# Performance work log

Hardware: AMD Instinct MI355X
Metric: run time of the kernel (lower is better)

Reference implementation:

```python
import jax, jax.numpy as jnp
import numpy as np

DIM = 768
HEADS = 12
HEAD_DIM = DIM // HEADS
B, N = 8, 1024


def setup_inputs() -> dict:
    key = jax.random.key(0)
    ks = jax.random.split(key, 5)
    x = jax.random.normal(ks[0], (B, N, DIM), dtype=jnp.float32)
    shared_rel_pos = jax.random.normal(ks[1], (HEADS, N, N), dtype=jnp.float32)
    qkv_w = jax.random.normal(ks[2], (3 * DIM, DIM), dtype=jnp.float32) * (DIM ** -0.5)
    proj_w = jax.random.normal(ks[3], (DIM, DIM), dtype=jnp.float32) * (DIM ** -0.5)
    proj_b = jnp.zeros((DIM,), dtype=jnp.float32)
    return {"x": x, "shared_rel_pos": shared_rel_pos, "qkv_w": qkv_w,
            "proj_w": proj_w, "proj_b": proj_b}


def reference(x, shared_rel_pos, qkv_w, proj_w, proj_b):
    Bt, Nt, C = x.shape
    scale = HEAD_DIM ** -0.5
    # qkv: Linear(dim, 3*dim, bias=False) -> (B, N, 3, H, hd) -> (3, B, H, N, hd)
    qkv = jnp.einsum('bnc,oc->bno', x, qkv_w)
    qkv = qkv.reshape(Bt, Nt, 3, HEADS, HEAD_DIM).transpose(2, 0, 3, 1, 4)
    q, k, v = qkv[0], qkv[1], qkv[2]
    # scaled dot-product attention with shared relative-position bias
    attn = jnp.einsum('bhqd,bhkd->bhqk', q, k) * scale
    attn = attn + shared_rel_pos[None]  # broadcast over batch
    attn = jax.nn.softmax(attn, axis=-1)
    out = jnp.einsum('bhqk,bhkd->bhqd', attn, v)
    out = out.transpose(0, 2, 1, 3).reshape(Bt, Nt, C)
    return jnp.einsum('bnc,oc->bno', out, proj_w) + proj_b
```

## Files before the change

kernel.cpp:

```cpp
#include <hip/hip_runtime.h>
#include <hip/hip_bf16.h>
#include <stdint.h>

#define HEADS 12
#define HD 64
#define SEQ 1024
#define CDIM 768

typedef __attribute__((ext_vector_type(8))) short bfrag;
typedef __attribute__((ext_vector_type(4))) float facc;

__device__ __forceinline__ ushort f2bf(float f) {
    union { float f; uint32_t u; } v; v.f = f;
    uint32_t u = v.u;
    uint32_t r = (u + 0x7FFFu + ((u >> 16) & 1u)) >> 16;
    return (ushort)r;
}
__device__ __forceinline__ float h2f(uint32_t u16) {
    union { _Float16 h; ushort u; } c; c.u = (ushort)u16; return (float)c.h;
}

__global__ void cvt_f32_bf16(const float* __restrict__ s, ushort* __restrict__ d, int n) {
    int i = (blockIdx.x * 256 + threadIdx.x) * 4;
    if (i + 3 < n) {
        float4 v = *(const float4*)(s + i);
        ushort4 o;
        o.x = f2bf(v.x); o.y = f2bf(v.y); o.z = f2bf(v.z); o.w = f2bf(v.w);
        *(ushort4*)(d + i) = o;
    }
}

__global__ void cvt_f32_f16(const float* __restrict__ s, ushort* __restrict__ d, int n) {
    int i = (blockIdx.x * 256 + threadIdx.x) * 4;
    if (i + 3 < n) {
        float4 v = *(const float4*)(s + i);
        union { _Float16 h; ushort u; } c0, c1, c2, c3;
        c0.h = (_Float16)v.x; c1.h = (_Float16)v.y;
        c2.h = (_Float16)v.z; c3.h = (_Float16)v.w;
        ushort4 o = {c0.u, c1.u, c2.u, c3.u};
        *(ushort4*)(d + i) = o;
    }
}

#define GLOAD16(gsrc, ldst) \
    __builtin_amdgcn_global_load_lds((const __attribute__((address_space(1))) uint32_t*)(gsrc), \
                                     (__attribute__((address_space(3))) uint32_t*)(ldst), 16, 0, 0)

template<int EPI>
__global__ __launch_bounds__(256) void gemm_nt(
    const ushort* __restrict__ A, const ushort* __restrict__ Bm,
    ushort* __restrict__ qb, ushort* __restrict__ kb, ushort* __restrict__ vb,
    const float* __restrict__ projb, float* __restrict__ out)
{
    __shared__ ushort As[128 * 32];
    __shared__ ushort Bs[128 * 32];
    const int t = threadIdx.x;
    const int w = t >> 6, l = t & 63;
    const int wm = w >> 1, wn = w & 1;
    const int lr = l & 15, lg = l >> 4;
    const int m0 = blockIdx.x * 128;
    const int o0 = blockIdx.y * 128;

    facc acc[4][4] = {};

    const int srow = w * 16 + (l >> 2);
    const int scol = (l & 3) * 8;
    const ushort* Ag = A + (size_t)(m0 + srow) * CDIM + scol;
    const ushort* Bg = Bm + (size_t)(o0 + srow) * CDIM + scol;

    for (int k0 = 0; k0 < CDIM; k0 += 32) {
        __syncthreads();
        GLOAD16(Ag + k0,             As + w * 512);
        GLOAD16(Ag + 64 * CDIM + k0, As + 2048 + w * 512);
        GLOAD16(Bg + k0,             Bs + w * 512);
        GLOAD16(Bg + 64 * CDIM + k0, Bs + 2048 + w * 512);
        __syncthreads();
        bfrag af[4], bf[4];
#pragma unroll
        for (int m = 0; m < 4; ++m)
            af[m] = *(const bfrag*)&As[(wm * 64 + m * 16 + lr) * 32 + lg * 8];
#pragma unroll
        for (int n = 0; n < 4; ++n)
            bf[n] = *(const bfrag*)&Bs[(wn * 64 + n * 16 + lr) * 32 + lg * 8];
#pragma unroll
        for (int m = 0; m < 4; ++m)
#pragma unroll
            for (int n = 0; n < 4; ++n)
                acc[m][n] = __builtin_amdgcn_mfma_f32_16x16x32_bf16(af[m], bf[n], acc[m][n], 0, 0, 0);
    }

    if (EPI == 0) {
        const int tsel = o0 / CDIM;
        const int h_base = (o0 % CDIM) / 64;
        ushort* dst = (tsel == 0) ? qb : ((tsel == 1) ? kb : vb);
        const float scl = (tsel == 0) ? 0.125f : 1.0f;
#pragma unroll
        for (int m = 0; m < 4; ++m) {
            int grow = m0 + wm * 64 + m * 16 + lg * 4;
#pragma unroll
            for (int n = 0; n < 4; ++n) {
                int h = h_base + wn;
                int d = n * 16 + lr;
#pragma unroll
                for (int r = 0; r < 4; ++r) {
                    int row = grow + r;
                    int b = row >> 10, nn = row & 1023;
                    dst[(((size_t)(b * HEADS + h)) * SEQ + nn) * HD + d] = f2bf(acc[m][n][r] * scl);
                }
            }
        }
    } else {
#pragma unroll
        for (int m = 0; m < 4; ++m) {
            int grow = m0 + wm * 64 + m * 16 + lg * 4;
#pragma unroll
            for (int n = 0; n < 4; ++n) {
                int o = o0 + wn * 64 + n * 16 + lr;
                float bias = projb[o];
#pragma unroll
                for (int r = 0; r < 4; ++r)
                    out[(size_t)(grow + r) * CDIM + o] = acc[m][n][r] + bias;
            }
        }
    }
}

__global__ __launch_bounds__(256, 3) void attn_kernel(
    const ushort* __restrict__ qbuf, const ushort* __restrict__ kbuf,
    const ushort* __restrict__ vbuf, const ushort* __restrict__ biash,
    ushort* __restrict__ attn_out)
{
    __shared__ ushort Ks[64 * 72];
    __shared__ ushort Vt[64 * 72];
    __shared__ ushort Ps[4][32 * 72];

    const int t = threadIdx.x;
    const int w = t >> 6, l = t & 63;
    const int lr = l & 15, lg = l >> 4;

    const int bid = blockIdx.x;
    const int lid = (bid & 7) * 96 + (bid >> 3);
    const int h  = lid >> 6;
    const int qt = (lid >> 3) & 7;
    const int b  = lid & 7;

    const int q0 = qt * 128;
    const size_t headoff = (size_t)(b * HEADS + h) * SEQ * HD;
    const int qrb = q0 + w * 32;

    bfrag aQ[2][2];
#pragma unroll
    for (int n = 0; n < 2; ++n) {
        const ushort* Qp = qbuf + headoff + (size_t)(qrb + n * 16 + lr) * HD;
        aQ[n][0] = *(const bfrag*)(Qp + lg * 8);
        aQ[n][1] = *(const bfrag*)(Qp + 32 + lg * 8);
    }

    float mrun[2] = {-1e30f, -1e30f}, lrun[2] = {0.0f, 0.0f};
    facc Ov[2][4] = {};

    const ushort* bprow[2];
#pragma unroll
    for (int n = 0; n < 2; ++n)
        bprow[n] = biash + ((size_t)h * SEQ + qrb + n * 16 + lr) * SEQ;

    const int krow = t >> 3, kc = (t & 7) * 8;
    const int p2 = t & 31, vg_ = t >> 5;
    const ushort* kgb = kbuf + headoff + (size_t)krow * HD + kc;
    const ushort* vgb = vbuf + headoff + (size_t)(2 * p2) * HD + vg_ * 8;

    bfrag krA = *(const bfrag*)(kgb);
    bfrag krB = *(const bfrag*)(kgb + (size_t)32 * HD);
    bfrag vrA = *(const bfrag*)(vgb);
    bfrag vrB = *(const bfrag*)(vgb + HD);
    uint2 bcur[2][4];
#pragma unroll
    for (int n = 0; n < 2; ++n)
#pragma unroll
        for (int c = 0; c < 4; ++c)
            bcur[n][c] = *(const uint2*)(bprow[n] + c * 16 + lg * 4);

    *(bfrag*)&Ks[krow * 72 + kc] = krA;
    *(bfrag*)&Ks[(krow + 32) * 72 + kc] = krB;
#pragma unroll
    for (int i = 0; i < 8; ++i) {
        uint32_t pk = (uint32_t)(uint16_t)vrA[i] | ((uint32_t)(uint16_t)vrB[i] << 16);
        *(uint32_t*)&Vt[(vg_ * 8 + i) * 72 + 2 * p2] = pk;
    }
    __syncthreads();

    for (int tt = 0; tt < 16; ++tt) {
        const int kv0 = tt << 6;
        uint2 bnxt[2][4];
        if (tt < 15) {
            const int kvn = kv0 + 64;
            krA = *(const bfrag*)(kgb + (size_t)kvn * HD);
            krB = *(const bfrag*)(kgb + (size_t)(kvn + 32) * HD);
            vrA = *(const bfrag*)(vgb + (size_t)kvn * HD);
            vrB = *(const bfrag*)(vgb + (size_t)(kvn + 1) * HD);
#pragma unroll
            for (int n = 0; n < 2; ++n)
#pragma unroll
                for (int c = 0; c < 4; ++c)
                    bnxt[n][c] = *(const uint2*)(bprow[n] + kvn + c * 16 + lg * 4);
        }

        facc St[2][4];
        __builtin_amdgcn_s_setprio(1);
#pragma unroll
        for (int c = 0; c < 4; ++c) {
            bfrag kf0 = *(const bfrag*)&Ks[(c * 16 + lr) * 72 + lg * 8];
            bfrag kf1 = *(const bfrag*)&Ks[(c * 16 + lr) * 72 + 32 + lg * 8];
#pragma unroll
            for (int n = 0; n < 2; ++n) {
                facc s = {};
                s = __builtin_amdgcn_mfma_f32_16x16x32_bf16(kf0, aQ[n][0], s, 0, 0, 0);
                s = __builtin_amdgcn_mfma_f32_16x16x32_bf16(kf1, aQ[n][1], s, 0, 0, 0);
                St[n][c] = s;
            }
        }
        __builtin_amdgcn_s_setprio(0);

#pragma unroll
        for (int n = 0; n < 2; ++n)
#pragma unroll
            for (int c = 0; c < 4; ++c) {
                uint2 bb = bcur[n][c];
                St[n][c][0] += h2f(bb.x & 0xffffu);
                St[n][c][1] += h2f(bb.x >> 16);
                St[n][c][2] += h2f(bb.y & 0xffffu);
                St[n][c][3] += h2f(bb.y >> 16);
            }

        float pmax[2];
#pragma unroll
        for (int n = 0; n < 2; ++n) {
            float m0 = fmaxf(fmaxf(St[n][0][0], St[n][0][1]), fmaxf(St[n][0][2], St[n][0][3]));
            float m1 = fmaxf(fmaxf(St[n][1][0], St[n][1][1]), fmaxf(St[n][1][2], St[n][1][3]));
            float m2 = fmaxf(fmaxf(St[n][2][0], St[n][2][1]), fmaxf(St[n][2][2], St[n][2][3]));
            float m3 = fmaxf(fmaxf(St[n][3][0], St[n][3][1]), fmaxf(St[n][3][2], St[n][3][3]));
            float mx = fmaxf(fmaxf(m0, m1), fmaxf(m2, m3));
            mx = fmaxf(mx, __shfl_xor(mx, 16));
            mx = fmaxf(mx, __shfl_xor(mx, 32));
            pmax[n] = mx;
        }

        int ok = (pmax[0] <= mrun[0] + 8.0f) && (pmax[1] <= mrun[1] + 8.0f);
        if (!__all(ok)) {
            float al[2];
#pragma unroll
            for (int n = 0; n < 2; ++n) {
                float mnew = fmaxf(mrun[n], pmax[n]);
                al[n] = __expf(mrun[n] - mnew);
                mrun[n] = mnew;
                lrun[n] *= al[n];
            }
#pragma unroll
            for (int n = 0; n < 2; ++n)
#pragma unroll
                for (int r = 0; r < 4; ++r) {
                    float a = __shfl(al[n], lg * 4 + r);
#pragma unroll
                    for (int d = 0; d < 4; ++d) Ov[n][d][r] *= a;
                }
        }

#pragma unroll
        for (int n = 0; n < 2; ++n) {
            float sum = 0.0f;
#pragma unroll
            for (int c = 0; c < 4; ++c) {
#pragma unroll
                for (int r = 0; r < 4; ++r) {
                    float p = __expf(St[n][c][r] - mrun[n]);
                    St[n][c][r] = p;
                    sum += p;
                }
                ushort4 pk = {f2bf(St[n][c][0]), f2bf(St[n][c][1]),
                              f2bf(St[n][c][2]), f2bf(St[n][c][3])};
                *(ushort4*)&Ps[w][(n * 16 + lr) * 72 + c * 16 + lg * 4] = pk;
            }
            sum += __shfl_xor(sum, 16);
            sum += __shfl_xor(sum, 32);
            lrun[n] += sum;
        }

        bfrag aP[2][2];
#pragma unroll
        for (int n = 0; n < 2; ++n) {
            aP[n][0] = *(const bfrag*)&Ps[w][(n * 16 + lr) * 72 + lg * 8];
            aP[n][1] = *(const bfrag*)&Ps[w][(n * 16 + lr) * 72 + 32 + lg * 8];
        }
        __builtin_amdgcn_s_setprio(1);
#pragma unroll
        for (int d = 0; d < 4; ++d) {
            bfrag bv0 = *(const bfrag*)&Vt[(d * 16 + lr) * 72 + lg * 8];
            bfrag bv1 = *(const bfrag*)&Vt[(d * 16 + lr) * 72 + 32 + lg * 8];
#pragma unroll
            for (int n = 0; n < 2; ++n) {
                Ov[n][d] = __builtin_amdgcn_mfma_f32_16x16x32_bf16(aP[n][0], bv0, Ov[n][d], 0, 0, 0);
                Ov[n][d] = __builtin_amdgcn_mfma_f32_16x16x32_bf16(aP[n][1], bv1, Ov[n][d], 0, 0, 0);
            }
        }
        __builtin_amdgcn_s_setprio(0);

        if (tt < 15) {
            __syncthreads();
            *(bfrag*)&Ks[krow * 72 + kc] = krA;
            *(bfrag*)&Ks[(krow + 32) * 72 + kc] = krB;
#pragma unroll
            for (int i = 0; i < 8; ++i) {
                uint32_t pk = (uint32_t)(uint16_t)vrA[i] | ((uint32_t)(uint16_t)vrB[i] << 16);
                *(uint32_t*)&Vt[(vg_ * 8 + i) * 72 + 2 * p2] = pk;
            }
#pragma unroll
            for (int n = 0; n < 2; ++n)
#pragma unroll
                for (int c = 0; c < 4; ++c)
                    bcur[n][c] = bnxt[n][c];
            __syncthreads();
        }
    }

#pragma unroll
    for (int n = 0; n < 2; ++n) {
        ushort* op = attn_out + ((size_t)b * SEQ + qrb + n * 16) * CDIM + h * HD;
#pragma unroll
        for (int r = 0; r < 4; ++r) {
            float ll = __shfl(lrun[n], lg * 4 + r);
            float rl = 1.0f / ll;
#pragma unroll
            for (int d = 0; d < 4; ++d)
                op[(size_t)(lg * 4 + r) * CDIM + d * 16 + lr] = f2bf(Ov[n][d][r] * rl);
        }
    }
}

extern "C" void kernel_launch(void* const* d_in, const int* in_sizes, int n_in,
                              void* d_out, int out_size, void* d_ws, size_t ws_size,
                              hipStream_t stream) {
    const float* x     = (const float*)d_in[0];
    const float* rel   = (const float*)d_in[1];
    const float* qkvw  = (const float*)d_in[2];
    const float* projw = (const float*)d_in[3];
    const float* projb = (const float*)d_in[4];
    float* out = (float*)d_out;

    char* ws = (char*)d_ws;
    ushort* biash = (ushort*)(ws);
    ushort* qb    = (ushort*)(ws + 25165824);
    ushort* kb    = (ushort*)(ws + 37748736);
    ushort* vb    = (ushort*)(ws + 50331648);
    ushort* attnb = (ushort*)(ws + 62914560);
    ushort* xbf   = attnb;
    ushort* wbf   = (ushort*)(ws + 75497472);
    ushort* pwbf  = (ushort*)(ws + 79036416);

    cvt_f32_bf16<<<6144, 256, 0, stream>>>(x, xbf, 6291456);
    cvt_f32_bf16<<<1728, 256, 0, stream>>>(qkvw, wbf, 1769472);
    cvt_f32_bf16<<<576, 256, 0, stream>>>(projw, pwbf, 589824);
    cvt_f32_f16<<<12288, 256, 0, stream>>>(rel, biash, 12582912);

    gemm_nt<0><<<dim3(64, 18), 256, 0, stream>>>(xbf, wbf, qb, kb, vb, nullptr, nullptr);
    attn_kernel<<<768, 256, 0, stream>>>(qb, kb, vb, biash, attnb);
    gemm_nt<1><<<dim3(64, 6), 256, 0, stream>>>(attnb, pwbf, nullptr, nullptr, nullptr, projb, out);
}
```

Before: 172.1 us.

## Double-buffer K/V tiles, keep P in registers, fold bias and exp2 scaling

```diff
diff --git a/kernel.cpp b/kernel.cpp
--- a/kernel.cpp
+++ b/kernel.cpp
@@ -9,6 +9,7 @@
 
 typedef __attribute__((ext_vector_type(8))) short bfrag;
 typedef __attribute__((ext_vector_type(4))) float facc;
+typedef __attribute__((ext_vector_type(4))) _Float16 h4;
 
 __device__ __forceinline__ ushort f2bf(float f) {
     union { float f; uint32_t u; } v; v.f = f;
@@ -16,29 +17,38 @@
     uint32_t r = (u + 0x7FFFu + ((u >> 16) & 1u)) >> 16;
     return (ushort)r;
 }
+__device__ __forceinline__ ushort f2h(float f) {
+    union { _Float16 h; ushort u; } c; c.h = (_Float16)f; return c.u;
+}
 __device__ __forceinline__ float h2f(uint32_t u16) {
     union { _Float16 h; ushort u; } c; c.u = (ushort)u16; return (float)c.h;
 }
 
-__global__ void cvt_f32_bf16(const float* __restrict__ s, ushort* __restrict__ d, int n) {
-    int i = (blockIdx.x * 256 + threadIdx.x) * 4;
-    if (i + 3 < n) {
-        float4 v = *(const float4*)(s + i);
-        ushort4 o;
-        o.x = f2bf(v.x); o.y = f2bf(v.y); o.z = f2bf(v.z); o.w = f2bf(v.w);
-        *(ushort4*)(d + i) = o;
-    }
-}
-
-__global__ void cvt_f32_f16(const float* __restrict__ s, ushort* __restrict__ d, int n) {
-    int i = (blockIdx.x * 256 + threadIdx.x) * 4;
-    if (i + 3 < n) {
-        float4 v = *(const float4*)(s + i);
-        union { _Float16 h; ushort u; } c0, c1, c2, c3;
-        c0.h = (_Float16)v.x; c1.h = (_Float16)v.y;
-        c2.h = (_Float16)v.z; c3.h = (_Float16)v.w;
-        ushort4 o = {c0.u, c1.u, c2.u, c3.u};
-        *(ushort4*)(d + i) = o;
+__global__ void cvt_all(const float* __restrict__ x, const float* __restrict__ qw,
+                        const float* __restrict__ pw, const float* __restrict__ rel,
+                        ushort* __restrict__ xd, ushort* __restrict__ qd,
+                        ushort* __restrict__ pd, ushort* __restrict__ rd) {
+    long i = ((long)blockIdx.x * 256 + threadIdx.x) * 4;
+    if (i < 6291456) {
+        float4 v = *(const float4*)(x + i);
+        ushort4 o = {f2bf(v.x), f2bf(v.y), f2bf(v.z), f2bf(v.w)};
+        *(ushort4*)(xd + i) = o;
+    } else if (i < 8060928) {
+        long j = i - 6291456;
+        float4 v = *(const float4*)(qw + j);
+        ushort4 o = {f2bf(v.x), f2bf(v.y), f2bf(v.z), f2bf(v.w)};
+        *(ushort4*)(qd + j) = o;
+    } else if (i < 8650752) {
+        long j = i - 8060928;
+        float4 v = *(const float4*)(pw + j);
+        ushort4 o = {f2bf(v.x), f2bf(v.y), f2bf(v.z), f2bf(v.w)};
+        *(ushort4*)(pd + j) = o;
+    } else {
+        long j = i - 8650752;
+        float4 v = *(const float4*)(rel + j);
+        ushort4 o = {f2h(v.x * 1.44269504f), f2h(v.y * 1.44269504f),
+                     f2h(v.z * 1.44269504f), f2h(v.w * 1.44269504f)};
+        *(ushort4*)(rd + j) = o;
     }
 }
 
@@ -93,7 +103,7 @@
         const int tsel = o0 / CDIM;
         const int h_base = (o0 % CDIM) / 64;
         ushort* dst = (tsel == 0) ? qb : ((tsel == 1) ? kb : vb);
-        const float scl = (tsel == 0) ? 0.125f : 1.0f;
+        const float scl = (tsel == 0) ? 0.18033688f : 1.0f;
 #pragma unroll
         for (int m = 0; m < 4; ++m) {
             int grow = m0 + wm * 64 + m * 16 + lg * 4;
@@ -105,7 +115,9 @@
                 for (int r = 0; r < 4; ++r) {
                     int row = grow + r;
                     int b = row >> 10, nn = row & 1023;
-                    dst[(((size_t)(b * HEADS + h)) * SEQ + nn) * HD + d] = f2bf(acc[m][n][r] * scl);
+                    ushort val = (tsel == 2) ? f2h(acc[m][n][r])
+                                             : f2bf(acc[m][n][r] * scl);
+                    dst[(((size_t)(b * HEADS + h)) * SEQ + nn) * HD + d] = val;
                 }
             }
         }
@@ -130,9 +142,8 @@
     const ushort* __restrict__ vbuf, const ushort* __restrict__ biash,
     ushort* __restrict__ attn_out)
 {
-    __shared__ ushort Ks[64 * 72];
-    __shared__ ushort Vt[64 * 72];
-    __shared__ ushort Ps[4][32 * 72];
+    __shared__ ushort Ks[2][64 * 72];
+    __shared__ ushort Vt[2][64 * 72];
 
     const int t = threadIdx.x;
     const int w = t >> 6, l = t & 63;
@@ -173,47 +184,45 @@
     bfrag krB = *(const bfrag*)(kgb + (size_t)32 * HD);
     bfrag vrA = *(const bfrag*)(vgb);
     bfrag vrB = *(const bfrag*)(vgb + HD);
-    uint2 bcur[2][4];
+    uint2 bcur[2][4], bnxt[2][4];
 #pragma unroll
     for (int n = 0; n < 2; ++n)
 #pragma unroll
         for (int c = 0; c < 4; ++c)
             bcur[n][c] = *(const uint2*)(bprow[n] + c * 16 + lg * 4);
 
-    *(bfrag*)&Ks[krow * 72 + kc] = krA;
-    *(bfrag*)&Ks[(krow + 32) * 72 + kc] = krB;
+    *(bfrag*)&Ks[0][krow * 72 + kc] = krA;
+    *(bfrag*)&Ks[0][(krow + 32) * 72 + kc] = krB;
 #pragma unroll
     for (int i = 0; i < 8; ++i) {
         uint32_t pk = (uint32_t)(uint16_t)vrA[i] | ((uint32_t)(uint16_t)vrB[i] << 16);
-        *(uint32_t*)&Vt[(vg_ * 8 + i) * 72 + 2 * p2] = pk;
-    }
+        *(uint32_t*)&Vt[0][(vg_ * 8 + i) * 72 + 2 * p2] = pk;
+    }
+    krA = *(const bfrag*)(kgb + (size_t)64 * HD);
+    krB = *(const bfrag*)(kgb + (size_t)96 * HD);
+    vrA = *(const bfrag*)(vgb + (size_t)64 * HD);
+    vrB = *(const bfrag*)(vgb + (size_t)65 * HD);
     __syncthreads();
 
     for (int tt = 0; tt < 16; ++tt) {
-        const int kv0 = tt << 6;
-        uint2 bnxt[2][4];
-        if (tt < 15) {
-            const int kvn = kv0 + 64;
-            krA = *(const bfrag*)(kgb + (size_t)kvn * HD);
-            krB = *(const bfrag*)(kgb + (size_t)(kvn + 32) * HD);
-            vrA = *(const bfrag*)(vgb + (size_t)kvn * HD);
-            vrB = *(const bfrag*)(vgb + (size_t)(kvn + 1) * HD);
-#pragma unroll
-            for (int n = 0; n < 2; ++n)
-#pragma unroll
-                for (int c = 0; c < 4; ++c)
-                    bnxt[n][c] = *(const uint2*)(bprow[n] + kvn + c * 16 + lg * 4);
-        }
+        const int cur = tt & 1;
+        const ushort* Kc = Ks[cur];
+        const ushort* Vc = Vt[cur];
 
         facc St[2][4];
         __builtin_amdgcn_s_setprio(1);
 #pragma unroll
         for (int c = 0; c < 4; ++c) {
-            bfrag kf0 = *(const bfrag*)&Ks[(c * 16 + lr) * 72 + lg * 8];
-            bfrag kf1 = *(const bfrag*)&Ks[(c * 16 + lr) * 72 + 32 + lg * 8];
+            bfrag kf0 = *(const bfrag*)&Kc[(c * 16 + lr) * 72 + lg * 8];
+            bfrag kf1 = *(const bfrag*)&Kc[(c * 16 + lr) * 72 + 32 + lg * 8];
 #pragma unroll
             for (int n = 0; n < 2; ++n) {
-                facc s = {};
+                uint2 bb = bcur[n][c];
+                facc s;
+                s[0] = h2f(bb.x & 0xffffu);
+                s[1] = h2f(bb.x >> 16);
+                s[2] = h2f(bb.y & 0xffffu);
+                s[3] = h2f(bb.y >> 16);
                 s = __builtin_amdgcn_mfma_f32_16x16x32_bf16(kf0, aQ[n][0], s, 0, 0, 0);
                 s = __builtin_amdgcn_mfma_f32_16x16x32_bf16(kf1, aQ[n][1], s, 0, 0, 0);
                 St[n][c] = s;
@@ -221,16 +230,14 @@
         }
         __builtin_amdgcn_s_setprio(0);
 
-#pragma unroll
-        for (int n = 0; n < 2; ++n)
-#pragma unroll
-            for (int c = 0; c < 4; ++c) {
-                uint2 bb = bcur[n][c];
-                St[n][c][0] += h2f(bb.x & 0xffffu);
-                St[n][c][1] += h2f(bb.x >> 16);
-                St[n][c][2] += h2f(bb.y & 0xffffu);
-                St[n][c][3] += h2f(bb.y >> 16);
-            }
+        if (tt < 15) {
+            const int kvn = (tt + 1) << 6;
+#pragma unroll
+            for (int n = 0; n < 2; ++n)
+#pragma unroll
+                for (int c = 0; c < 4; ++c)
+                    bnxt[n][c] = *(const uint2*)(bprow[n] + kvn + c * 16 + lg * 4);
+        }
 
         float pmax[2];
 #pragma unroll
@@ -245,13 +252,13 @@
             pmax[n] = mx;
         }
 
-        int ok = (pmax[0] <= mrun[0] + 8.0f) && (pmax[1] <= mrun[1] + 8.0f);
+        int ok = (pmax[0] <= mrun[0] + 11.541560f) && (pmax[1] <= mrun[1] + 11.541560f);
         if (!__all(ok)) {
             float al[2];
 #pragma unroll
             for (int n = 0; n < 2; ++n) {
                 float mnew = fmaxf(mrun[n], pmax[n]);
-                al[n] = __expf(mrun[n] - mnew);
+                al[n] = exp2f(mrun[n] - mnew);
                 mrun[n] = mnew;
                 lrun[n] *= al[n];
             }
@@ -265,6 +272,7 @@
                 }
         }
 
+        h4 pf[2][4];
 #pragma unroll
         for (int n = 0; n < 2; ++n) {
             float sum = 0.0f;
@@ -272,53 +280,53 @@
             for (int c = 0; c < 4; ++c) {
 #pragma unroll
                 for (int r = 0; r < 4; ++r) {
-                    float p = __expf(St[n][c][r] - mrun[n]);
-                    St[n][c][r] = p;
+                    float p = exp2f(St[n][c][r] - mrun[n]);
                     sum += p;
+                    pf[n][c][r] = (_Float16)p;
                 }
-                ushort4 pk = {f2bf(St[n][c][0]), f2bf(St[n][c][1]),
-                              f2bf(St[n][c][2]), f2bf(St[n][c][3])};
-                *(ushort4*)&Ps[w][(n * 16 + lr) * 72 + c * 16 + lg * 4] = pk;
             }
             sum += __shfl_xor(sum, 16);
             sum += __shfl_xor(sum, 32);
             lrun[n] += sum;
         }
 
-        bfrag aP[2][2];
-#pragma unroll
-        for (int n = 0; n < 2; ++n) {
-            aP[n][0] = *(const bfrag*)&Ps[w][(n * 16 + lr) * 72 + lg * 8];
-            aP[n][1] = *(const bfrag*)&Ps[w][(n * 16 + lr) * 72 + 32 + lg * 8];
-        }
+        if (tt < 15) {
+            *(bfrag*)&Ks[cur ^ 1][krow * 72 + kc] = krA;
+            *(bfrag*)&Ks[cur ^ 1][(krow + 32) * 72 + kc] = krB;
+#pragma unroll
+            for (int i = 0; i < 8; ++i) {
+                uint32_t pk = (uint32_t)(uint16_t)vrA[i] | ((uint32_t)(uint16_t)vrB[i] << 16);
+                *(uint32_t*)&Vt[cur ^ 1][(vg_ * 8 + i) * 72 + 2 * p2] = pk;
+            }
+        }
+        if (tt < 14) {
+            const int kvn = (tt + 2) << 6;
+            krA = *(const bfrag*)(kgb + (size_t)kvn * HD);
+            krB = *(const bfrag*)(kgb + (size_t)(kvn + 32) * HD);
+            vrA = *(const bfrag*)(vgb + (size_t)kvn * HD);
+            vrB = *(const bfrag*)(vgb + (size_t)(kvn + 1) * HD);
+        }
+
         __builtin_amdgcn_s_setprio(1);
 #pragma unroll
-        for (int d = 0; d < 4; ++d) {
-            bfrag bv0 = *(const bfrag*)&Vt[(d * 16 + lr) * 72 + lg * 8];
-            bfrag bv1 = *(const bfrag*)&Vt[(d * 16 + lr) * 72 + 32 + lg * 8];
-#pragma unroll
-            for (int n = 0; n < 2; ++n) {
-                Ov[n][d] = __builtin_amdgcn_mfma_f32_16x16x32_bf16(aP[n][0], bv0, Ov[n][d], 0, 0, 0);
-                Ov[n][d] = __builtin_amdgcn_mfma_f32_16x16x32_bf16(aP[n][1], bv1, Ov[n][d], 0, 0, 0);
+        for (int d0 = 0; d0 < 4; ++d0) {
+#pragma unroll
+            for (int c = 0; c < 4; ++c) {
+                h4 bv = *(const h4*)&Vc[(d0 * 16 + lr) * 72 + c * 16 + lg * 4];
+#pragma unroll
+                for (int n = 0; n < 2; ++n)
+                    Ov[n][d0] = __builtin_amdgcn_mfma_f32_16x16x16f16(pf[n][c], bv, Ov[n][d0], 0, 0, 0);
             }
         }
         __builtin_amdgcn_s_setprio(0);
 
         if (tt < 15) {
             __syncthreads();
-            *(bfrag*)&Ks[krow * 72 + kc] = krA;
-            *(bfrag*)&Ks[(krow + 32) * 72 + kc] = krB;
-#pragma unroll
-            for (int i = 0; i < 8; ++i) {
-                uint32_t pk = (uint32_t)(uint16_t)vrA[i] | ((uint32_t)(uint16_t)vrB[i] << 16);
-                *(uint32_t*)&Vt[(vg_ * 8 + i) * 72 + 2 * p2] = pk;
-            }
 #pragma unroll
             for (int n = 0; n < 2; ++n)
 #pragma unroll
                 for (int c = 0; c < 4; ++c)
                     bcur[n][c] = bnxt[n][c];
-            __syncthreads();
         }
     }
 
@@ -356,10 +364,7 @@
     ushort* wbf   = (ushort*)(ws + 75497472);
     ushort* pwbf  = (ushort*)(ws + 79036416);
 
-    cvt_f32_bf16<<<6144, 256, 0, stream>>>(x, xbf, 6291456);
-    cvt_f32_bf16<<<1728, 256, 0, stream>>>(qkvw, wbf, 1769472);
-    cvt_f32_bf16<<<576, 256, 0, stream>>>(projw, pwbf, 589824);
-    cvt_f32_f16<<<12288, 256, 0, stream>>>(rel, biash, 12582912);
+    cvt_all<<<20736, 256, 0, stream>>>(x, qkvw, projw, rel, xbf, wbf, pwbf, biash);
 
     gemm_nt<0><<<dim3(64, 18), 256, 0, stream>>>(xbf, wbf, qb, kb, vb, nullptr, nullptr);
     attn_kernel<<<768, 256, 0, stream>>>(qb, kb, vb, biash, attnb);
```

Result: faster. 155.2 us (-9.8%).
